# Performance work log

Hardware: AMD Instinct MI355X
Metric: run time of the kernel (lower is better)

## Reference

```python
import jax, jax.numpy as jnp
import numpy as np

IN_DIM = 256
OUT_DIM = 64
N = 8192
ALPHA = 0.2  # LeakyReLU negative slope
NEG_BIG = -9e15


def setup_inputs() -> dict:
    key = jax.random.key(0)
    k_h, k_A, k_W, k_a = jax.random.split(key, 4)
    h = jax.random.normal(k_h, (N, IN_DIM), dtype=jnp.float32)
    A = jax.random.randint(k_A, (N, N), 0, 2, dtype=jnp.int32)
    # xavier_uniform with gain=1.414
    gain = 1.414
    lim_W = gain * np.sqrt(6.0 / (IN_DIM + OUT_DIM))
    W = jax.random.uniform(k_W, (IN_DIM, OUT_DIM), minval=-lim_W, maxval=lim_W, dtype=jnp.float32)
    lim_a = gain * np.sqrt(6.0 / (2 * OUT_DIM + 1))
    a = jax.random.uniform(k_a, (2 * OUT_DIM, 1), minval=-lim_a, maxval=lim_a, dtype=jnp.float32)
    return {"h": h, "A": A, "W": W, "a": a}


def reference(h, A, W, a):
    # Wh: [N, d]
    Wh = h @ W
    # e_ij = leakyrelu([Wh_i || Wh_j] . a) = leakyrelu(Wh_i.a1 + Wh_j.a2)
    # -> avoid the O(N^2 * 2d) concat; compute rank-1 decomposition directly.
    a1 = a[:OUT_DIM, 0]   # [d]
    a2 = a[OUT_DIM:, 0]   # [d]
    f1 = Wh @ a1          # [N] contribution of source node i
    f2 = Wh @ a2          # [N] contribution of target node j
    e = jax.nn.leaky_relu(f1[:, None] + f2[None, :], negative_slope=ALPHA)  # [N, N]
    e = jnp.where(A > 0, e, NEG_BIG)
    attention = jax.nn.softmax(e, axis=1)  # [N, N]
    # dropout=0.0 (eval mode): identity
    h_prime = attention @ Wh               # [N, d]
    return jax.nn.elu(h_prime)             # concat=True -> ELU
```

## Files before the change

### kernel.cpp

```cpp
#include <hip/hip_runtime.h>
#include <math.h>
#include <stdint.h>

#define NV 8192
#define KD 256
#define DD 64
#define ALPHA 0.2f
#define TI 64
#define CJ 128
#define BLK 512

typedef _Float16 half8 __attribute__((ext_vector_type(8)));
typedef float floatx4 __attribute__((ext_vector_type(4)));

#define OFF_WHT  0
#define OFF_F1   (DD * NV / 2)
#define OFF_F2   (OFF_F1 + NV)
#define OFF_PACC (OFF_F2 + NV)

__global__ __launch_bounds__(256) void gat_pre(
    const float* __restrict__ h, const float* __restrict__ W,
    const float* __restrict__ a, ushort* __restrict__ whT,
    float* __restrict__ f1, float* __restrict__ f2) {
  __shared__ float hrow[4][KD];
  __shared__ __align__(8) ushort tw[DD][4];
  const int wv = threadIdx.x >> 6, lane = threadIdx.x & 63;
  const int i = blockIdx.x * 4 + wv;
  *(float4*)&hrow[wv][lane * 4] = *(const float4*)&h[(long long)i * KD + lane * 4];
  __syncthreads();
  float wh = 0.f;
#pragma unroll 8
  for (int c = 0; c < KD; ++c) wh += hrow[wv][c] * W[c * DD + lane];
  float p1 = wh * a[lane];
  float p2 = wh * a[DD + lane];
#pragma unroll
  for (int off = 32; off > 0; off >>= 1) {
    p1 += __shfl_down(p1, off);
    p2 += __shfl_down(p2, off);
  }
  if (lane == 0) { f1[i] = p1; f2[i] = p2; }
  union { _Float16 hf; ushort u; } cv;
  cv.hf = (_Float16)wh;
  tw[lane][wv] = cv.u;
  __syncthreads();
  if (threadIdx.x < DD) {
    *(uint2*)&whT[(long long)threadIdx.x * NV + blockIdx.x * 4] = *(uint2*)&tw[threadIdx.x][0];
  }
}

__global__ __launch_bounds__(BLK) void gat_main(
    const int* __restrict__ A, const ushort* __restrict__ whT,
    const float* __restrict__ f1, const float* __restrict__ f2,
    float* __restrict__ pacc, float* __restrict__ pl, int S) {
  __shared__ __align__(16) ushort w_lds[TI * CJ];
  __shared__ __align__(16) ushort b_lds[TI * CJ];
  __shared__ float f1_lds[TI], M_lds[TI], redf[8];

  const int tid = threadIdx.x;
  const int wave = tid >> 6, lane = tid & 63;
  const int tile = blockIdx.x & 127;
  const int s = blockIdx.x >> 7;
  const int i0 = tile * TI;
  const int jrange = NV / S;
  const int j0 = s * jrange;

  float m = -1e30f;
#pragma unroll
  for (int q = 0; q < 16; ++q) m = fmaxf(m, f2[tid + q * BLK]);
#pragma unroll
  for (int off = 32; off > 0; off >>= 1) m = fmaxf(m, __shfl_down(m, off));
  if (lane == 0) redf[wave] = m;
  __syncthreads();
  if (tid < TI) {
    float mm = redf[0];
#pragma unroll
    for (int k = 1; k < 8; ++k) mm = fmaxf(mm, redf[k]);
    float v = f1[i0 + tid];
    f1_lds[tid] = v;
    float x = v + mm;
    M_lds[tid] = x > 0.f ? x : ALPHA * x;
  }

  const int c4 = (tid & 31) * 4;
  const int k8w = (tid & 31) >> 1;
  const int sub = (tid & 1) * 8;
  const int rb = tid >> 5;
  const int mt = wave >> 1;
  const int nt0 = (wave & 1) * 2;
  const int m_ = lane & 15, quad = lane >> 4;

  floatx4 acc0 = {0.f, 0.f, 0.f, 0.f}, acc1 = {0.f, 0.f, 0.f, 0.f};
  float lp[4] = {0.f, 0.f, 0.f, 0.f};

  const int nch = jrange / CJ;
  for (int ch = 0; ch < nch; ++ch) {
    const int jb = j0 + ch * CJ;
    __syncthreads();

#pragma unroll
    for (int u = 0; u < 2; ++u) {
      const int idx = tid + u * BLK;
      const int n = idx >> 4, c = idx & 15;
      const uint4 t = *(const uint4*)(whT + (long long)n * NV + jb + 8 * (c ^ (n & 15)));
      *(uint4*)&b_lds[idx * 8] = t;
    }

    const float4 f2v = *(const float4*)(f2 + jb + c4);
#pragma unroll
    for (int p = 0; p < 4; ++p) {
      const int r = rb + 16 * p;
      const int4 a4 = *(const int4*)(A + (long long)(i0 + r) * NV + jb + c4);
      const float f1r = f1_lds[r], Mr = M_lds[r];
      float w0, w1, w2, w3;
      { float x = f1r + f2v.x; x = x > 0.f ? x : ALPHA * x; w0 = (a4.x > 0) ? __expf(x - Mr) : 0.f; }
      { float x = f1r + f2v.y; x = x > 0.f ? x : ALPHA * x; w1 = (a4.y > 0) ? __expf(x - Mr) : 0.f; }
      { float x = f1r + f2v.z; x = x > 0.f ? x : ALPHA * x; w2 = (a4.z > 0) ? __expf(x - Mr) : 0.f; }
      { float x = f1r + f2v.w; x = x > 0.f ? x : ALPHA * x; w3 = (a4.w > 0) ? __expf(x - Mr) : 0.f; }
      union { _Float16 hf[4]; uint2 u2; } pk;
      pk.hf[0] = (_Float16)w0; pk.hf[1] = (_Float16)w1;
      pk.hf[2] = (_Float16)w2; pk.hf[3] = (_Float16)w3;
      lp[p] += (float)pk.hf[0] + (float)pk.hf[1] + (float)pk.hf[2] + (float)pk.hf[3];
      *(uint2*)((char*)w_lds + (r * 16 + (k8w ^ (r & 15))) * 16 + sub) = pk.u2;
    }
    __syncthreads();

#pragma unroll
    for (int ks = 0; ks < 4; ++ks) {
      const int cc = 4 * ks + quad;
      const half8 af = *(const half8*)((const char*)w_lds + (((16 * mt + m_) * 16) + (cc ^ m_)) * 16);
      const half8 b0 = *(const half8*)((const char*)b_lds + (((16 * nt0 + m_) * 16) + (cc ^ m_)) * 16);
      const half8 b1 = *(const half8*)((const char*)b_lds + (((16 * (nt0 + 1) + m_) * 16) + (cc ^ m_)) * 16);
      acc0 = __builtin_amdgcn_mfma_f32_16x16x32_f16(af, b0, acc0, 0, 0, 0);
      acc1 = __builtin_amdgcn_mfma_f32_16x16x32_f16(af, b1, acc1, 0, 0, 0);
    }
  }

#pragma unroll
  for (int p = 0; p < 4; ++p) {
    float v = lp[p];
    v += __shfl_down(v, 16, 32);
    v += __shfl_down(v, 8, 32);
    v += __shfl_down(v, 4, 32);
    v += __shfl_down(v, 2, 32);
    v += __shfl_down(v, 1, 32);
    if ((tid & 31) == 0) pl[(long long)s * NV + i0 + rb + 16 * p] = v;
  }

#pragma unroll
  for (int reg = 0; reg < 4; ++reg) {
    const int i = i0 + 16 * mt + quad * 4 + reg;
    const long long base = ((long long)s * NV + i) * DD + m_;
    pacc[base + 16 * nt0] = acc0[reg];
    pacc[base + 16 * (nt0 + 1)] = acc1[reg];
  }
}

__global__ __launch_bounds__(256) void gat_fin(const float* __restrict__ pacc,
                                               const float* __restrict__ pl,
                                               float* __restrict__ out, int S) {
  const int idx = blockIdx.x * 256 + threadIdx.x;
  const int i = idx >> 6;
  float sum = 0.f, l = 0.f;
  for (int q = 0; q < S; ++q) sum += pacc[(long long)q * (NV * DD) + idx];
  for (int q = 0; q < S; ++q) l += pl[q * NV + i];
  const float v = sum / l;
  out[idx] = v > 0.f ? v : expm1f(v);
}

extern "C" void kernel_launch(void* const* d_in, const int* in_sizes, int n_in,
                              void* d_out, int out_size, void* d_ws, size_t ws_size,
                              hipStream_t stream) {
  const float* h = (const float*)d_in[0];
  const int* A = (const int*)d_in[1];
  const float* W = (const float*)d_in[2];
  const float* a = (const float*)d_in[3];
  float* out = (float*)d_out;
  float* ws = (float*)d_ws;

  ushort* whT = (ushort*)(ws + OFF_WHT);
  float* f1 = ws + OFF_F1;
  float* f2 = ws + OFF_F2;
  float* pacc = ws + OFF_PACC;

  int S = 4;
  while (S > 1 &&
         (size_t)(OFF_PACC + (size_t)S * (NV * DD + NV)) * sizeof(float) > ws_size)
    S >>= 1;
  float* pl = pacc + (size_t)S * NV * DD;

  gat_pre<<<NV / 4, 256, 0, stream>>>(h, W, a, whT, f1, f2);
  gat_main<<<(NV / TI) * S, BLK, 0, stream>>>(A, whT, f1, f2, pacc, pl, S);
  gat_fin<<<NV * DD / 256, 256, 0, stream>>>(pacc, pl, out, S);
}
```

Measured before the change: 396.8 us.

## Prefetch next chunk into registers, raise split count, batch rows in pre kernel

The main kernel now loads the next chunk's adjacency, Wh-transpose and f2 values into registers while the current chunk is computed, overlapping global latency with exp and MFMA work at the cost of more registers. The j-split count goes from 4 to 8 to launch more blocks for occupancy, which adds partial-sum traffic in the finish kernel. The pre kernel handles 16 rows per block and reuses each W load across 4 rows, with wider transposed stores.

```diff
diff --git a/kernel.cpp b/kernel.cpp
--- a/kernel.cpp
+++ b/kernel.cpp
@@ -22,29 +22,44 @@
     const float* __restrict__ h, const float* __restrict__ W,
     const float* __restrict__ a, ushort* __restrict__ whT,
     float* __restrict__ f1, float* __restrict__ f2) {
-  __shared__ float hrow[4][KD];
-  __shared__ __align__(8) ushort tw[DD][4];
-  const int wv = threadIdx.x >> 6, lane = threadIdx.x & 63;
-  const int i = blockIdx.x * 4 + wv;
-  *(float4*)&hrow[wv][lane * 4] = *(const float4*)&h[(long long)i * KD + lane * 4];
+  __shared__ float hrow[16][KD];
+  __shared__ ushort tw[DD][20];
+  const int tid = threadIdx.x;
+  const int i0 = blockIdx.x * 16;
+#pragma unroll
+  for (int u = 0; u < 4; ++u) {
+    const int idx = tid + u * 256;
+    const int row = idx >> 6, col = (idx & 63) * 4;
+    *(float4*)&hrow[row][col] = *(const float4*)&h[(long long)(i0 + row) * KD + col];
+  }
   __syncthreads();
-  float wh = 0.f;
-#pragma unroll 8
-  for (int c = 0; c < KD; ++c) wh += hrow[wv][c] * W[c * DD + lane];
-  float p1 = wh * a[lane];
-  float p2 = wh * a[DD + lane];
-#pragma unroll
-  for (int off = 32; off > 0; off >>= 1) {
-    p1 += __shfl_down(p1, off);
-    p2 += __shfl_down(p2, off);
-  }
-  if (lane == 0) { f1[i] = p1; f2[i] = p2; }
-  union { _Float16 hf; ushort u; } cv;
-  cv.hf = (_Float16)wh;
-  tw[lane][wv] = cv.u;
+  const int d = tid & 63;
+  const int rg = tid >> 6;
+  float wh[4] = {0.f, 0.f, 0.f, 0.f};
+#pragma unroll 4
+  for (int c = 0; c < KD; ++c) {
+    const float wc = W[c * DD + d];
+#pragma unroll
+    for (int r = 0; r < 4; ++r) wh[r] += hrow[rg * 4 + r][c] * wc;
+  }
+  const float a1 = a[d], a2 = a[DD + d];
+#pragma unroll
+  for (int r = 0; r < 4; ++r) {
+    float p1 = wh[r] * a1, p2 = wh[r] * a2;
+#pragma unroll
+    for (int off = 32; off > 0; off >>= 1) {
+      p1 += __shfl_down(p1, off);
+      p2 += __shfl_down(p2, off);
+    }
+    if (d == 0) { f1[i0 + rg * 4 + r] = p1; f2[i0 + rg * 4 + r] = p2; }
+    union { _Float16 hf; ushort u; } cv;
+    cv.hf = (_Float16)wh[r];
+    tw[d][rg * 4 + r] = cv.u;
+  }
   __syncthreads();
-  if (threadIdx.x < DD) {
-    *(uint2*)&whT[(long long)threadIdx.x * NV + blockIdx.x * 4] = *(uint2*)&tw[threadIdx.x][0];
+  if (tid < 128) {
+    const int dd = tid >> 1, hf = tid & 1;
+    *(uint4*)&whT[(long long)dd * NV + i0 + hf * 8] = *(uint4*)&tw[dd][hf * 8];
   }
 }
 
@@ -85,6 +100,8 @@
   const int k8w = (tid & 31) >> 1;
   const int sub = (tid & 1) * 8;
   const int rb = tid >> 5;
+  const int bn0 = tid >> 4, bc0 = tid & 15;
+  const int bn1 = (tid + BLK) >> 4, bc1 = tid & 15;
   const int mt = wave >> 1;
   const int nt0 = (wave & 1) * 2;
   const int m_ = lane & 15, quad = lane >> 4;
@@ -92,30 +109,46 @@
   floatx4 acc0 = {0.f, 0.f, 0.f, 0.f}, acc1 = {0.f, 0.f, 0.f, 0.f};
   float lp[4] = {0.f, 0.f, 0.f, 0.f};
 
+  int4 a_cur[4], a_nxt[4];
+  uint4 b_cur[2], b_nxt[2];
+  float4 f2_cur, f2_nxt;
+
+  {
+    const int jb = j0;
+#pragma unroll
+    for (int p = 0; p < 4; ++p)
+      a_cur[p] = *(const int4*)(A + (long long)(i0 + rb + 16 * p) * NV + jb + c4);
+    b_cur[0] = *(const uint4*)(whT + (long long)bn0 * NV + jb + 8 * (bc0 ^ (bn0 & 15)));
+    b_cur[1] = *(const uint4*)(whT + (long long)bn1 * NV + jb + 8 * (bc1 ^ (bn1 & 15)));
+    f2_cur = *(const float4*)(f2 + jb + c4);
+  }
+
   const int nch = jrange / CJ;
   for (int ch = 0; ch < nch; ++ch) {
-    const int jb = j0 + ch * CJ;
+    if (ch + 1 < nch) {
+      const int jb = j0 + (ch + 1) * CJ;
+#pragma unroll
+      for (int p = 0; p < 4; ++p)
+        a_nxt[p] = *(const int4*)(A + (long long)(i0 + rb + 16 * p) * NV + jb + c4);
+      b_nxt[0] = *(const uint4*)(whT + (long long)bn0 * NV + jb + 8 * (bc0 ^ (bn0 & 15)));
+      b_nxt[1] = *(const uint4*)(whT + (long long)bn1 * NV + jb + 8 * (bc1 ^ (bn1 & 15)));
+      f2_nxt = *(const float4*)(f2 + jb + c4);
+    }
     __syncthreads();
 
-#pragma unroll
-    for (int u = 0; u < 2; ++u) {
-      const int idx = tid + u * BLK;
-      const int n = idx >> 4, c = idx & 15;
-      const uint4 t = *(const uint4*)(whT + (long long)n * NV + jb + 8 * (c ^ (n & 15)));
-      *(uint4*)&b_lds[idx * 8] = t;
-    }
-
-    const float4 f2v = *(const float4*)(f2 + jb + c4);
+    *(uint4*)&b_lds[(tid) * 8] = b_cur[0];
+    *(uint4*)&b_lds[(tid + BLK) * 8] = b_cur[1];
+
 #pragma unroll
     for (int p = 0; p < 4; ++p) {
       const int r = rb + 16 * p;
-      const int4 a4 = *(const int4*)(A + (long long)(i0 + r) * NV + jb + c4);
+      const int4 a4 = a_cur[p];
       const float f1r = f1_lds[r], Mr = M_lds[r];
       float w0, w1, w2, w3;
-      { float x = f1r + f2v.x; x = x > 0.f ? x : ALPHA * x; w0 = (a4.x > 0) ? __expf(x - Mr) : 0.f; }
-      { float x = f1r + f2v.y; x = x > 0.f ? x : ALPHA * x; w1 = (a4.y > 0) ? __expf(x - Mr) : 0.f; }
-      { float x = f1r + f2v.z; x = x > 0.f ? x : ALPHA * x; w2 = (a4.z > 0) ? __expf(x - Mr) : 0.f; }
-      { float x = f1r + f2v.w; x = x > 0.f ? x : ALPHA * x; w3 = (a4.w > 0) ? __expf(x - Mr) : 0.f; }
+      { float x = f1r + f2_cur.x; x = x > 0.f ? x : ALPHA * x; w0 = (a4.x > 0) ? __expf(x - Mr) : 0.f; }
+      { float x = f1r + f2_cur.y; x = x > 0.f ? x : ALPHA * x; w1 = (a4.y > 0) ? __expf(x - Mr) : 0.f; }
+      { float x = f1r + f2_cur.z; x = x > 0.f ? x : ALPHA * x; w2 = (a4.z > 0) ? __expf(x - Mr) : 0.f; }
+      { float x = f1r + f2_cur.w; x = x > 0.f ? x : ALPHA * x; w3 = (a4.w > 0) ? __expf(x - Mr) : 0.f; }
       union { _Float16 hf[4]; uint2 u2; } pk;
       pk.hf[0] = (_Float16)w0; pk.hf[1] = (_Float16)w1;
       pk.hf[2] = (_Float16)w2; pk.hf[3] = (_Float16)w3;
@@ -133,6 +166,11 @@
       acc0 = __builtin_amdgcn_mfma_f32_16x16x32_f16(af, b0, acc0, 0, 0, 0);
       acc1 = __builtin_amdgcn_mfma_f32_16x16x32_f16(af, b1, acc1, 0, 0, 0);
     }
+
+#pragma unroll
+    for (int p = 0; p < 4; ++p) a_cur[p] = a_nxt[p];
+    b_cur[0] = b_nxt[0]; b_cur[1] = b_nxt[1];
+    f2_cur = f2_nxt;
   }
 
 #pragma unroll
@@ -182,13 +220,13 @@
   float* f2 = ws + OFF_F2;
   float* pacc = ws + OFF_PACC;
 
-  int S = 4;
+  int S = 8;
   while (S > 1 &&
          (size_t)(OFF_PACC + (size_t)S * (NV * DD + NV)) * sizeof(float) > ws_size)
     S >>= 1;
   float* pl = pacc + (size_t)S * NV * DD;
 
-  gat_pre<<<NV / 4, 256, 0, stream>>>(h, W, a, whT, f1, f2);
+  gat_pre<<<NV / 16, 256, 0, stream>>>(h, W, a, whT, f1, f2);
   gat_main<<<(NV / TI) * S, BLK, 0, stream>>>(A, whT, f1, f2, pacc, pl, S);
   gat_fin<<<NV * DD / 256, 256, 0, stream>>>(pacc, pl, out, S);
 }
```

New measurement: 460.4 us. 16.0% more time.
